# Kernel optimization log

Hardware: AMD Instinct MI355X
Metric: run time of the kernel (lower is better)

The kernel has to match this reference:

```python
import jax, jax.numpy as jnp
import numpy as np


def setup_inputs() -> dict:
    key = jax.random.key(0)
    k1, k2 = jax.random.split(key)
    B, S_ENC, S_DEC, D = 8, 4096, 4096, 256
    enc_output = jax.random.normal(k1, (B, S_ENC, D), dtype=jnp.float32)
    dec_output = jax.random.normal(k2, (B, S_DEC, D), dtype=jnp.float32)
    return {"enc_output": enc_output, "dec_output": dec_output}


def reference(enc_output, dec_output):
    # a_t[b, i, j] = <enc[b, i], dec[b, j]>  -> [B, S_enc, S_dec]
    a_t = jnp.einsum('bid,bjd->bij', enc_output, dec_output)
    # softmax over encoder positions (axis=1), matching torch.softmax(a_t, dim=1)
    a_t = jax.nn.softmax(a_t, axis=1)
    # c_t[b, j, d] = sum_i a_t[b, i, j] * enc[b, i, d]  -> [B, S_dec, D]
    c_t = jnp.einsum('bij,bid->bjd', a_t, enc_output)
    return c_t
```

## Files before the change

kernel.cpp:

```cpp
#include <hip/hip_runtime.h>

typedef unsigned short u16;
typedef unsigned int u32;
typedef __attribute__((ext_vector_type(8))) _Float16 half8;
typedef __attribute__((ext_vector_type(2))) __fp16 fp16x2;
typedef __attribute__((ext_vector_type(16))) float f32x16;

#define MFMA32(A, B, C) __builtin_amdgcn_mfma_f32_32x32x16_f16(A, B, C, 0, 0, 0)

constexpr int BN = 8;
constexpr int S = 4096;
constexpr int D = 256;
constexpr int KB = 32;
constexpr int NT = S / KB;
constexpr int TILE_U16 = KB * D;
constexpr int TP_U16 = 2 * TILE_U16;

__device__ __forceinline__ u32 pk2h(float a, float b) {
  union { _Float16 h[2]; u32 u; } x;
  x.h[0] = (_Float16)a; x.h[1] = (_Float16)b;
  return x.u;
}

__device__ __forceinline__ u32 pkrtz(float a, float b) {
  union { fp16x2 h; u32 u; } x;
  x.h = __builtin_amdgcn_cvt_pkrtz(a, b);
  return x.u;
}

__device__ __forceinline__ void gload_lds16(const void* g, void* l) {
  __builtin_amdgcn_global_load_lds((__attribute__((address_space(1))) void*)(void*)g,
                                   (__attribute__((address_space(3))) void*)l, 16, 0, 0);
}

__global__ __launch_bounds__(256) void convert_enc(const float* __restrict__ enc,
                                                   u16* __restrict__ ws) {
  const int blk = blockIdx.x;
  const int b = blk & 7;
  const int tp = blk >> 3;
  const int tid = threadIdx.x;

  const float* encb = enc + (size_t)b * S * D;

#pragma unroll
  for (int it = 0; it < 8; ++it) {
    int gg = it * 256 + tid;
    int t = tp * 2 + (gg >> 10);
    int g = gg & 1023;
    int i = g & 31;
    int ch = g >> 5;
    int d0 = ch * 8;
    const float* src = encb + (size_t)(t * 32 + i) * D + d0;
    float4 x = *(const float4*)src;
    float4 y = *(const float4*)(src + 4);
    uint4 o;
    o.x = pk2h(x.x, x.y); o.y = pk2h(x.z, x.w);
    o.z = pk2h(y.x, y.y); o.w = pk2h(y.z, y.w);
    *(uint4*)(ws + (size_t)(b * NT + t) * TP_U16 + g * 8) = o;
  }

  {
    int t = tp * 2 + (tid >> 7);
    int r = tid & 127;
    int o = r >> 5;
    int e = r & 31;
    int i0 = o * 8;
    int d0 = e * 8;
    float v[8][8];
#pragma unroll
    for (int rr = 0; rr < 8; ++rr) {
      const float* src = encb + (size_t)(t * 32 + i0 + rr) * D + d0;
      *(float4*)&v[rr][0] = *(const float4*)src;
      *(float4*)&v[rr][4] = *(const float4*)(src + 4);
    }
    int dsub = e >> 2;
    u16* dst = ws + (size_t)(b * NT + t) * TP_U16 + TILE_U16 +
               ((dsub * 4 + o) * 32 + (e & 3) * 8) * 8;
#pragma unroll
    for (int k = 0; k < 8; ++k) {
      uint4 q;
      q.x = pk2h(v[0][k], v[1][k]); q.y = pk2h(v[2][k], v[3][k]);
      q.z = pk2h(v[4][k], v[5][k]); q.w = pk2h(v[6][k], v[7][k]);
      *(uint4*)(dst + k * 8) = q;
    }
  }
}

__global__ __launch_bounds__(512, 2) void attn_kernel(const u16* __restrict__ ws_img,
                                                      const float* __restrict__ dec,
                                                      float* __restrict__ out) {
  __shared__ u16 lds[2][2][TP_U16];

  const int tid = threadIdx.x;
  const int w = tid >> 6;
  const int wq = w & 3;
  const int kh = w >> 2;
  const int lane = tid & 63;
  const int h = lane >> 5;
  const int l31 = lane & 31;

  const int blk = blockIdx.x;
  const int b = blk & 7;
  const int q0 = (blk >> 3) << 7;
  const int qw = q0 + wq * 32;

  const u16* packs = ws_img + (size_t)b * NT * TP_U16;
  const float* decb = dec + (size_t)b * S * D;

  const float LOG2E = 1.4426950408889634f;
  half8 qf[16];
#pragma unroll
  for (int c = 0; c < 16; ++c) {
    const float* p = decb + (size_t)(qw + l31) * D + c * 16 + h * 8;
    float4 x = *(const float4*)p;
    float4 y = *(const float4*)(p + 4);
    union { u32 u[4]; half8 v; } uu;
    uu.u[0] = pk2h(x.x * LOG2E, x.y * LOG2E);
    uu.u[1] = pk2h(x.z * LOG2E, x.w * LOG2E);
    uu.u[2] = pk2h(y.x * LOG2E, y.y * LOG2E);
    uu.u[3] = pk2h(y.z * LOG2E, y.w * LOG2E);
    qf[c] = uu.v;
  }

  f32x16 acc[8] = {};
  float mrun = -1e30f;
  float lrun = 0.f;

  auto stagef = [&](int buf, int t) {
    const char* gs = (const char*)(packs + (size_t)t * TP_U16) + wq * 8192 + lane * 16;
    char* ls = (char*)&lds[kh][buf][0] + wq * 8192;
#pragma unroll
    for (int it = 0; it < 8; ++it)
      gload_lds16(gs + it * 1024, ls + it * 1024);
  };

  auto qkf = [&](int buf) -> f32x16 {
    f32x16 s0 = {}, s1 = {};
    const char* eb = (const char*)&lds[kh][buf][0];
    __builtin_amdgcn_s_setprio(1);
#pragma unroll
    for (int c = 0; c < 16; c += 2) {
      half8 a0 = *(const half8*)(eb + ((c + 0) * 2 + h) * 512 + l31 * 16);
      half8 a1 = *(const half8*)(eb + ((c + 1) * 2 + h) * 512 + l31 * 16);
      s0 = MFMA32(a0, qf[c + 0], s0);
      s1 = MFMA32(a1, qf[c + 1], s1);
    }
    __builtin_amdgcn_s_setprio(0);
    return s0 + s1;
  };

  auto smpv = [&](const f32x16& st, int buf) {
    float x0 = fmaxf(fmaxf(st[0], st[1]), fmaxf(st[2], st[3]));
    float x1 = fmaxf(fmaxf(st[4], st[5]), fmaxf(st[6], st[7]));
    float x2 = fmaxf(fmaxf(st[8], st[9]), fmaxf(st[10], st[11]));
    float x3 = fmaxf(fmaxf(st[12], st[13]), fmaxf(st[14], st[15]));
    float tm = fmaxf(fmaxf(x0, x1), fmaxf(x2, x3));
    tm = fmaxf(tm, __shfl_xor(tm, 32));
    if (__any(tm > mrun + 11.5f)) {
      float mnew = fmaxf(mrun, tm);
      float alpha = __builtin_amdgcn_exp2f(mrun - mnew);
      mrun = mnew;
      lrun *= alpha;
#pragma unroll
      for (int ds = 0; ds < 8; ++ds)
#pragma unroll
        for (int r = 0; r < 16; ++r) acc[ds][r] *= alpha;
    }
    float p[16];
#pragma unroll
    for (int r = 0; r < 16; ++r) p[r] = __builtin_amdgcn_exp2f(st[r] - mrun);
    float y0 = (p[0] + p[1]) + (p[2] + p[3]);
    float y1 = (p[4] + p[5]) + (p[6] + p[7]);
    float y2 = (p[8] + p[9]) + (p[10] + p[11]);
    float y3 = (p[12] + p[13]) + (p[14] + p[15]);
    float rs = (y0 + y1) + (y2 + y3);
    rs += __shfl_xor(rs, 32);
    lrun += rs;

    u32 pkw[8];
#pragma unroll
    for (int rq = 0; rq < 4; ++rq) {
      pkw[rq * 2 + 0] = pkrtz(p[rq * 4 + 0], p[rq * 4 + 1]);
      pkw[rq * 2 + 1] = pkrtz(p[rq * 4 + 2], p[rq * 4 + 3]);
    }
    half8 bfr[2];
#pragma unroll
    for (int ic = 0; ic < 2; ++ic) {
      u32 own0 = pkw[(2 * ic + h) * 2 + 0];
      u32 own1 = pkw[(2 * ic + h) * 2 + 1];
      u32 send0 = pkw[(2 * ic + 1 - h) * 2 + 0];
      u32 send1 = pkw[(2 * ic + 1 - h) * 2 + 1];
      u32 r0 = (u32)__shfl_xor((int)send0, 32);
      u32 r1 = (u32)__shfl_xor((int)send1, 32);
      union { u32 u[4]; half8 v; } bb;
      bb.u[0] = h ? r0 : own0;
      bb.u[1] = h ? r1 : own1;
      bb.u[2] = h ? own0 : r0;
      bb.u[3] = h ? own1 : r1;
      bfr[ic] = bb.v;
    }

    const char* tb = (const char*)&lds[kh][buf][0] + TILE_U16 * 2;
    __builtin_amdgcn_s_setprio(1);
#pragma unroll
    for (int ic = 0; ic < 2; ++ic) {
#pragma unroll
      for (int ds = 0; ds < 8; ++ds) {
        half8 vf = *(const half8*)(tb + ((ds * 2 + ic) * 2 + h) * 512 + l31 * 16);
        acc[ds] = MFMA32(vf, bfr[ic], acc[ds]);
      }
    }
    __builtin_amdgcn_s_setprio(0);
  };

  f32x16 stp;

  stagef(0, kh);
  __syncthreads();

  if (kh == 0) {
    __syncthreads();
    stagef(1, 2); stp = qkf(0);
    __syncthreads();
  } else {
    stagef(1, 3); stp = qkf(0);
    __syncthreads();
    smpv(stp, 0);
    __syncthreads();
  }

#pragma unroll 1
  for (int j = 1; j < 64; ++j) {
    if (kh == 0) {
      smpv(stp, (j - 1) & 1);
      __syncthreads();
      if (j <= 62) stagef((j + 1) & 1, 2 * (j + 1));
      stp = qkf(j & 1);
      __syncthreads();
    } else {
      if (j <= 62) stagef((j + 1) & 1, 2 * (j + 1) + 1);
      stp = qkf(j & 1);
      __syncthreads();
      smpv(stp, j & 1);
      __syncthreads();
    }
  }

  if (kh == 0) {
    smpv(stp, 1);
    __syncthreads();
    __syncthreads();
  } else {
    __syncthreads();
    __syncthreads();
  }

  float* fb = (float*)&lds[0][0][0];
  constexpr int XS = 20;
  float* mlb = fb + 30208;

  if (kh == 1) {
    if (lane < 32) {
      mlb[wq * 64 + lane] = mrun;
      mlb[wq * 64 + 32 + lane] = lrun;
    }
#pragma unroll
    for (int d4 = 0; d4 < 4; ++d4) {
      float* dst = fb + ((wq * 4 + d4) * 64 + lane) * XS;
#pragma unroll
      for (int r4 = 0; r4 < 4; ++r4) {
        float4 v;
        v.x = acc[d4][r4 * 4 + 0]; v.y = acc[d4][r4 * 4 + 1];
        v.z = acc[d4][r4 * 4 + 2]; v.w = acc[d4][r4 * 4 + 3];
        *(float4*)(dst + r4 * 4) = v;
      }
    }
  }
  __syncthreads();

  float a0 = 0.f, a1 = 0.f, inv = 0.f;
  const int q = qw + l31;
  float* orow = out + ((size_t)(b * S + q)) * D;
  if (kh == 0) {
    float m1 = mlb[wq * 64 + l31];
    float l1 = mlb[wq * 64 + 32 + l31];
    float mn = fmaxf(mrun, m1);
    a0 = __builtin_amdgcn_exp2f(mrun - mn);
    a1 = __builtin_amdgcn_exp2f(m1 - mn);
    inv = 1.0f / (a0 * lrun + a1 * l1);
#pragma unroll
    for (int d4 = 0; d4 < 4; ++d4) {
      const float* src = fb + ((wq * 4 + d4) * 64 + lane) * XS;
#pragma unroll
      for (int rq = 0; rq < 4; ++rq) {
        float4 u = *(const float4*)(src + rq * 4);
        int d = d4 * 32 + rq * 8 + h * 4;
        float4 o;
        o.x = (a0 * acc[d4][rq * 4 + 0] + a1 * u.x) * inv;
        o.y = (a0 * acc[d4][rq * 4 + 1] + a1 * u.y) * inv;
        o.z = (a0 * acc[d4][rq * 4 + 2] + a1 * u.z) * inv;
        o.w = (a0 * acc[d4][rq * 4 + 3] + a1 * u.w) * inv;
        *(float4*)(orow + d) = o;
      }
    }
  }
  __syncthreads();

  if (kh == 1) {
#pragma unroll
    for (int d4 = 0; d4 < 4; ++d4) {
      float* dst = fb + ((wq * 4 + d4) * 64 + lane) * XS;
#pragma unroll
      for (int r4 = 0; r4 < 4; ++r4) {
        float4 v;
        v.x = acc[d4 + 4][r4 * 4 + 0]; v.y = acc[d4 + 4][r4 * 4 + 1];
        v.z = acc[d4 + 4][r4 * 4 + 2]; v.w = acc[d4 + 4][r4 * 4 + 3];
        *(float4*)(dst + r4 * 4) = v;
      }
    }
  }
  __syncthreads();

  if (kh == 0) {
#pragma unroll
    for (int d4 = 0; d4 < 4; ++d4) {
      const float* src = fb + ((wq * 4 + d4) * 64 + lane) * XS;
#pragma unroll
      for (int rq = 0; rq < 4; ++rq) {
        float4 u = *(const float4*)(src + rq * 4);
        int d = (d4 + 4) * 32 + rq * 8 + h * 4;
        float4 o;
        o.x = (a0 * acc[d4 + 4][rq * 4 + 0] + a1 * u.x) * inv;
        o.y = (a0 * acc[d4 + 4][rq * 4 + 1] + a1 * u.y) * inv;
        o.z = (a0 * acc[d4 + 4][rq * 4 + 2] + a1 * u.z) * inv;
        o.w = (a0 * acc[d4 + 4][rq * 4 + 3] + a1 * u.w) * inv;
        *(float4*)(orow + d) = o;
      }
    }
  }
}

extern "C" void kernel_launch(void* const* d_in, const int* in_sizes, int n_in,
                              void* d_out, int out_size, void* d_ws, size_t ws_size,
                              hipStream_t stream) {
  const float* enc = (const float*)d_in[0];
  const float* dec = (const float*)d_in[1];
  float* out = (float*)d_out;

  u16* ws_img = (u16*)d_ws;

  convert_enc<<<BN * (S / 64), 256, 0, stream>>>(enc, ws_img);
  attn_kernel<<<BN * (S / 128), 512, 0, stream>>>(ws_img, dec, out);
}
```

Before: 215.2 us.

## Replace warp-group ping-pong with in-wave QK/PV software pipeline and triple-buffered V

The two warp groups no longer alternate softmax and MFMA phases in staggered lockstep. Each wave now overlaps its QK^T for tile j with the PV accumulation for tile j-1, using probabilities packed in the previous iteration. K tiles are double-buffered and V tiles triple-buffered in a 160KB LDS array, which drops to one barrier per iteration. The setprio hints are removed. The change relies on the compiler interleaving the exp/softmax VALU work with independent MFMAs inside one wave, and it uses the full LDS budget.

```diff
diff --git a/kernel.cpp b/kernel.cpp
--- a/kernel.cpp
+++ b/kernel.cpp
@@ -89,7 +89,7 @@
 __global__ __launch_bounds__(512, 2) void attn_kernel(const u16* __restrict__ ws_img,
                                                       const float* __restrict__ dec,
                                                       float* __restrict__ out) {
-  __shared__ u16 lds[2][2][TP_U16];
+  __shared__ u16 LDSA[2][5][TILE_U16];
 
   const int tid = threadIdx.x;
   const int w = tid >> 6;
@@ -126,136 +126,124 @@
   float mrun = -1e30f;
   float lrun = 0.f;
 
-  auto stagef = [&](int buf, int t) {
-    const char* gs = (const char*)(packs + (size_t)t * TP_U16) + wq * 8192 + lane * 16;
-    char* ls = (char*)&lds[kh][buf][0] + wq * 8192;
+  auto stagef = [&](int t, int eslot, int tslot) {
+    const char* gs = (const char*)(packs + (size_t)t * TP_U16) +
+                     (wq >> 1) * 16384 + (wq & 1) * 8192 + lane * 16;
+    char* ls = (char*)&LDSA[kh][(wq < 2) ? eslot : (2 + tslot)][0] + (wq & 1) * 8192;
 #pragma unroll
     for (int it = 0; it < 8; ++it)
       gload_lds16(gs + it * 1024, ls + it * 1024);
   };
 
-  auto qkf = [&](int buf) -> f32x16 {
+  half8 bfrA[2];
+  half8 bfrB[2];
+
+  int e_cur = 0;
+  int t_prev = 2, t_cur = 0, t_next = 1;
+
+  stagef(kh, 0, 0);
+  __syncthreads();
+
+#pragma unroll 1
+  for (int j = 0; j < 64; ++j) {
+    if (j < 63) stagef(2 * (j + 1) + kh, e_cur ^ 1, t_next);
+
     f32x16 s0 = {}, s1 = {};
-    const char* eb = (const char*)&lds[kh][buf][0];
-    __builtin_amdgcn_s_setprio(1);
-#pragma unroll
-    for (int c = 0; c < 16; c += 2) {
-      half8 a0 = *(const half8*)(eb + ((c + 0) * 2 + h) * 512 + l31 * 16);
-      half8 a1 = *(const half8*)(eb + ((c + 1) * 2 + h) * 512 + l31 * 16);
-      s0 = MFMA32(a0, qf[c + 0], s0);
-      s1 = MFMA32(a1, qf[c + 1], s1);
-    }
-    __builtin_amdgcn_s_setprio(0);
-    return s0 + s1;
-  };
-
-  auto smpv = [&](const f32x16& st, int buf) {
-    float x0 = fmaxf(fmaxf(st[0], st[1]), fmaxf(st[2], st[3]));
-    float x1 = fmaxf(fmaxf(st[4], st[5]), fmaxf(st[6], st[7]));
-    float x2 = fmaxf(fmaxf(st[8], st[9]), fmaxf(st[10], st[11]));
-    float x3 = fmaxf(fmaxf(st[12], st[13]), fmaxf(st[14], st[15]));
-    float tm = fmaxf(fmaxf(x0, x1), fmaxf(x2, x3));
-    tm = fmaxf(tm, __shfl_xor(tm, 32));
-    if (__any(tm > mrun + 11.5f)) {
-      float mnew = fmaxf(mrun, tm);
-      float alpha = __builtin_amdgcn_exp2f(mrun - mnew);
-      mrun = mnew;
-      lrun *= alpha;
-#pragma unroll
-      for (int ds = 0; ds < 8; ++ds)
-#pragma unroll
-        for (int r = 0; r < 16; ++r) acc[ds][r] *= alpha;
-    }
-    float p[16];
-#pragma unroll
-    for (int r = 0; r < 16; ++r) p[r] = __builtin_amdgcn_exp2f(st[r] - mrun);
-    float y0 = (p[0] + p[1]) + (p[2] + p[3]);
-    float y1 = (p[4] + p[5]) + (p[6] + p[7]);
-    float y2 = (p[8] + p[9]) + (p[10] + p[11]);
-    float y3 = (p[12] + p[13]) + (p[14] + p[15]);
-    float rs = (y0 + y1) + (y2 + y3);
-    rs += __shfl_xor(rs, 32);
-    lrun += rs;
-
-    u32 pkw[8];
-#pragma unroll
-    for (int rq = 0; rq < 4; ++rq) {
-      pkw[rq * 2 + 0] = pkrtz(p[rq * 4 + 0], p[rq * 4 + 1]);
-      pkw[rq * 2 + 1] = pkrtz(p[rq * 4 + 2], p[rq * 4 + 3]);
-    }
-    half8 bfr[2];
-#pragma unroll
-    for (int ic = 0; ic < 2; ++ic) {
-      u32 own0 = pkw[(2 * ic + h) * 2 + 0];
-      u32 own1 = pkw[(2 * ic + h) * 2 + 1];
-      u32 send0 = pkw[(2 * ic + 1 - h) * 2 + 0];
-      u32 send1 = pkw[(2 * ic + 1 - h) * 2 + 1];
-      u32 r0 = (u32)__shfl_xor((int)send0, 32);
-      u32 r1 = (u32)__shfl_xor((int)send1, 32);
-      union { u32 u[4]; half8 v; } bb;
-      bb.u[0] = h ? r0 : own0;
-      bb.u[1] = h ? r1 : own1;
-      bb.u[2] = h ? own0 : r0;
-      bb.u[3] = h ? own1 : r1;
-      bfr[ic] = bb.v;
-    }
-
-    const char* tb = (const char*)&lds[kh][buf][0] + TILE_U16 * 2;
-    __builtin_amdgcn_s_setprio(1);
+    {
+      const char* eb = (const char*)&LDSA[kh][e_cur][0];
+#pragma unroll
+      for (int c = 0; c < 16; c += 2) {
+        half8 a0 = *(const half8*)(eb + ((c + 0) * 2 + h) * 512 + l31 * 16);
+        half8 a1 = *(const half8*)(eb + ((c + 1) * 2 + h) * 512 + l31 * 16);
+        s0 = MFMA32(a0, qf[c + 0], s0);
+        s1 = MFMA32(a1, qf[c + 1], s1);
+      }
+    }
+
+    if (j > 0) {
+      const char* tb = (const char*)&LDSA[kh][2 + t_prev][0];
+#pragma unroll
+      for (int ic = 0; ic < 2; ++ic) {
+#pragma unroll
+        for (int ds = 0; ds < 8; ++ds) {
+          half8 vf = *(const half8*)(tb + ((ds * 2 + ic) * 2 + h) * 512 + l31 * 16);
+          acc[ds] = MFMA32(vf, bfrA[ic], acc[ds]);
+        }
+      }
+    }
+
+    {
+      f32x16 st = s0 + s1;
+      float x0 = fmaxf(fmaxf(st[0], st[1]), fmaxf(st[2], st[3]));
+      float x1 = fmaxf(fmaxf(st[4], st[5]), fmaxf(st[6], st[7]));
+      float x2 = fmaxf(fmaxf(st[8], st[9]), fmaxf(st[10], st[11]));
+      float x3 = fmaxf(fmaxf(st[12], st[13]), fmaxf(st[14], st[15]));
+      float tm = fmaxf(fmaxf(x0, x1), fmaxf(x2, x3));
+      tm = fmaxf(tm, __shfl_xor(tm, 32));
+      if (__any(tm > mrun + 11.5f)) {
+        float mnew = fmaxf(mrun, tm);
+        float alpha = __builtin_amdgcn_exp2f(mrun - mnew);
+        mrun = mnew;
+        lrun *= alpha;
+#pragma unroll
+        for (int ds = 0; ds < 8; ++ds)
+#pragma unroll
+          for (int r = 0; r < 16; ++r) acc[ds][r] *= alpha;
+      }
+#pragma unroll
+      for (int r = 0; r < 16; ++r) st[r] = __builtin_amdgcn_exp2f(st[r] - mrun);
+      float y0 = (st[0] + st[1]) + (st[2] + st[3]);
+      float y1 = (st[4] + st[5]) + (st[6] + st[7]);
+      float y2 = (st[8] + st[9]) + (st[10] + st[11]);
+      float y3 = (st[12] + st[13]) + (st[14] + st[15]);
+      float rs = (y0 + y1) + (y2 + y3);
+      rs += __shfl_xor(rs, 32);
+      lrun += rs;
+
+      u32 pkw[8];
+#pragma unroll
+      for (int rq = 0; rq < 4; ++rq) {
+        pkw[rq * 2 + 0] = pkrtz(st[rq * 4 + 0], st[rq * 4 + 1]);
+        pkw[rq * 2 + 1] = pkrtz(st[rq * 4 + 2], st[rq * 4 + 3]);
+      }
+#pragma unroll
+      for (int ic = 0; ic < 2; ++ic) {
+        u32 own0 = pkw[(2 * ic + h) * 2 + 0];
+        u32 own1 = pkw[(2 * ic + h) * 2 + 1];
+        u32 send0 = pkw[(2 * ic + 1 - h) * 2 + 0];
+        u32 send1 = pkw[(2 * ic + 1 - h) * 2 + 1];
+        u32 r0 = (u32)__shfl_xor((int)send0, 32);
+        u32 r1 = (u32)__shfl_xor((int)send1, 32);
+        union { u32 u[4]; half8 v; } bb;
+        bb.u[0] = h ? r0 : own0;
+        bb.u[1] = h ? r1 : own1;
+        bb.u[2] = h ? own0 : r0;
+        bb.u[3] = h ? own1 : r1;
+        bfrB[ic] = bb.v;
+      }
+    }
+
+    __syncthreads();
+
+    bfrA[0] = bfrB[0]; bfrA[1] = bfrB[1];
+    e_cur ^= 1;
+    t_prev = t_cur; t_cur = t_next; t_next = (t_next == 2) ? 0 : t_next + 1;
+  }
+
+  {
+    const char* tb = (const char*)&LDSA[kh][2 + t_prev][0];
 #pragma unroll
     for (int ic = 0; ic < 2; ++ic) {
 #pragma unroll
       for (int ds = 0; ds < 8; ++ds) {
         half8 vf = *(const half8*)(tb + ((ds * 2 + ic) * 2 + h) * 512 + l31 * 16);
-        acc[ds] = MFMA32(vf, bfr[ic], acc[ds]);
-      }
-    }
-    __builtin_amdgcn_s_setprio(0);
-  };
-
-  f32x16 stp;
-
-  stagef(0, kh);
-  __syncthreads();
-
-  if (kh == 0) {
-    __syncthreads();
-    stagef(1, 2); stp = qkf(0);
-    __syncthreads();
-  } else {
-    stagef(1, 3); stp = qkf(0);
-    __syncthreads();
-    smpv(stp, 0);
-    __syncthreads();
-  }
-
-#pragma unroll 1
-  for (int j = 1; j < 64; ++j) {
-    if (kh == 0) {
-      smpv(stp, (j - 1) & 1);
-      __syncthreads();
-      if (j <= 62) stagef((j + 1) & 1, 2 * (j + 1));
-      stp = qkf(j & 1);
-      __syncthreads();
-    } else {
-      if (j <= 62) stagef((j + 1) & 1, 2 * (j + 1) + 1);
-      stp = qkf(j & 1);
-      __syncthreads();
-      smpv(stp, j & 1);
-      __syncthreads();
-    }
-  }
-
-  if (kh == 0) {
-    smpv(stp, 1);
-    __syncthreads();
-    __syncthreads();
-  } else {
-    __syncthreads();
-    __syncthreads();
-  }
-
-  float* fb = (float*)&lds[0][0][0];
+        acc[ds] = MFMA32(vf, bfrA[ic], acc[ds]);
+      }
+    }
+  }
+  __syncthreads();
+
+  float* fb = (float*)&LDSA[0][0][0];
   constexpr int XS = 20;
   float* mlb = fb + 30208;
 
```

Result: faster. 192.5 us (-10.5%).
